# Kernel optimization log

Measured on AMD Instinct MI355X. Metric: run time of the kernel, lower is better.

## Reference

```python
import jax, jax.numpy as jnp
import numpy as np
import math

B, S, DIM = 2, 2048, 1024
H, KVH = 16, 4
HD = DIM // H          # 64, head dim
WINDOW = 256           # sliding-window size (0 = global)
ROPE_BASE = 10000.0
EPS = 1e-6


def setup_inputs() -> dict:
    key = jax.random.key(0)
    ks = jax.random.split(key, 6)
    s = 0.02
    return {
        "x": jax.random.normal(ks[0], (B, S, DIM), jnp.float32),
        "Wq": jax.random.normal(ks[1], (DIM, DIM), jnp.float32) * s,
        "Wk": jax.random.normal(ks[2], (KVH * HD, DIM), jnp.float32) * s,
        "Wv": jax.random.normal(ks[3], (KVH * HD, DIM), jnp.float32) * s,
        "Wo": jax.random.normal(ks[4], (DIM, DIM), jnp.float32) * s,
        "q_gain": jnp.ones((H,), jnp.float32),
        "pair_mix": jnp.tile(jnp.eye(2, dtype=jnp.float32), (H // 2, 1, 1))
                    + 0.01 * jax.random.normal(ks[5], (H // 2, 2, 2), jnp.float32),
    }


def _rms_norm(v):
    # F.rms_norm over last dim, no learned weight
    return v * jax.lax.rsqrt(jnp.mean(v * v, axis=-1, keepdims=True) + EPS)


def _rope_tables(seqlen, dtype):
    inv_freq = 1.0 / (ROPE_BASE ** (jnp.arange(0, HD, 2, dtype=jnp.float32) / HD))  # [HD/2]
    t = jnp.arange(seqlen, dtype=jnp.float32)
    freqs = jnp.outer(t, inv_freq)                        # [S, HD/2]
    return jnp.cos(freqs).astype(dtype)[None, None], jnp.sin(freqs).astype(dtype)[None, None]


def _apply_rotary(v, cos, sin):
    half = v.shape[-1] // 2
    v1, v2 = v[..., :half], v[..., half:]
    return jnp.concatenate((v1 * cos + v2 * sin, -v1 * sin + v2 * cos), axis=-1)


def reference(x, Wq, Wk, Wv, Wo, q_gain, pair_mix):
    bsz, seqlen, dim = x.shape
    q = (x @ Wq.T).reshape(bsz, seqlen, H, HD).transpose(0, 2, 1, 3)    # [B,H,S,D]
    k = (x @ Wk.T).reshape(bsz, seqlen, KVH, HD).transpose(0, 2, 1, 3)  # [B,KV,S,D]
    v = (x @ Wv.T).reshape(bsz, seqlen, KVH, HD).transpose(0, 2, 1, 3)

    q = _rms_norm(q)
    k = _rms_norm(k)
    cos, sin = _rope_tables(seqlen, q.dtype)
    q = _apply_rotary(q, cos, sin)
    k = _apply_rotary(k, cos, sin)
    q = q * q_gain.astype(q.dtype)[None, :, None, None]

    # GQA expansion (repeat_interleave over head axis)
    rep = H // KVH
    k_full = jnp.repeat(k, rep, axis=1)  # [B,H,S,D]
    v_full = jnp.repeat(v, rep, axis=1)

    # sliding-window causal mask: attend iff 0 <= i-j < WINDOW
    pos = jnp.arange(seqlen)
    mask = (pos[:, None] >= pos[None, :]) & (pos[:, None] - pos[None, :] < WINDOW)

    scale = 1.0 / math.sqrt(HD)
    scores = jnp.einsum('bhqd,bhkd->bhqk', q, k_full) * scale
    scores = jnp.where(mask[None, None], scores, jnp.finfo(scores.dtype).min)
    att = jax.nn.softmax(scores, axis=-1)
    y = jnp.einsum('bhqk,bhkd->bhqd', att, v_full)  # [B,H,S,D]

    # paired-head mixing: mix each consecutive head pair with a 2x2 matrix
    yp = y.reshape(bsz, H // 2, 2, seqlen, HD)
    y = jnp.einsum('bpitd,poi->bpotd', yp, pair_mix.astype(y.dtype)).reshape(bsz, H, seqlen, HD)

    out = y.transpose(0, 2, 1, 3).reshape(bsz, seqlen, dim) @ Wo.T
    return out
```

## Files before the change

kernel.cpp:

```cpp
#include <hip/hip_runtime.h>
#include <hip/hip_bf16.h>
#include <cstdint>

#define S_LEN 2048
#define QKV_COLS 1536

typedef __bf16 bf16_t;
typedef bf16_t bf16x8 __attribute__((ext_vector_type(8)));
typedef bf16_t bf16x4 __attribute__((ext_vector_type(4)));
typedef float f32x4 __attribute__((ext_vector_type(4)));

typedef __attribute__((address_space(1))) void as1_void;
typedef __attribute__((address_space(3))) void as3_void;

__device__ __forceinline__ void async_load16(const void* g, void* lds) {
  __builtin_amdgcn_global_load_lds(
      (as1_void*)(uintptr_t)g,
      (as3_void*)(uint32_t)(uintptr_t)lds,
      16, 0, 0);
}

__device__ __forceinline__ uint32_t pkbf(float a, float b) {
  union { bf16_t h[2]; uint32_t u; } c;
  c.h[0] = (bf16_t)a; c.h[1] = (bf16_t)b;
  return c.u;
}

__global__ __launch_bounds__(256) void convert_all(
    const float4* __restrict__ x, const float4* __restrict__ wq,
    const float4* __restrict__ wk, const float4* __restrict__ wv,
    const float4* __restrict__ wo, const float* __restrict__ pm,
    bf16x4* __restrict__ xb, bf16x4* __restrict__ wqkvb, bf16x4* __restrict__ wob) {
  int u = blockIdx.x * 256 + threadIdx.x;
  if (u >= 1441792) {
    int off = u - 1441792;
    int flat = off * 4;
    int row = flat >> 10, colf = flat & 1023;
    int col2p = colf & ~64;
    int p = colf >> 7, ii = (colf >> 6) & 1;
    float4 a = wo[(row * 1024 + col2p) >> 2];
    float4 bq = wo[(row * 1024 + (col2p | 64)) >> 2];
    float m0v = pm[p * 4 + ii], m1v = pm[p * 4 + 2 + ii];
    bf16x4 o4;
    o4[0] = (bf16_t)(m0v * a.x + m1v * bq.x);
    o4[1] = (bf16_t)(m0v * a.y + m1v * bq.y);
    o4[2] = (bf16_t)(m0v * a.z + m1v * bq.z);
    o4[3] = (bf16_t)(m0v * a.w + m1v * bq.w);
    wob[off] = o4;
    return;
  }
  const float4* src; bf16x4* dst; int off;
  if (u < 1048576)      { src = x;  dst = xb;             off = u; }
  else if (u < 1310720) { src = wq; dst = wqkvb;          off = u - 1048576; }
  else if (u < 1376256) { src = wk; dst = wqkvb + 262144; off = u - 1310720; }
  else                  { src = wv; dst = wqkvb + 327680; off = u - 1376256; }
  float4 f = src[off];
  bf16x4 o;
  o[0] = (bf16_t)f.x; o[1] = (bf16_t)f.y; o[2] = (bf16_t)f.z; o[3] = (bf16_t)f.w;
  dst[off] = o;
}

__global__ __launch_bounds__(256) void gemm_qkv(
    const bf16_t* __restrict__ A, const bf16_t* __restrict__ B,
    bf16_t* __restrict__ C, bf16_t* __restrict__ vt,
    const float* __restrict__ q_gain, int N, int K) {
  __shared__ bf16_t As[2][64 * 64];
  __shared__ bf16_t Bs[2][128 * 64];
  const int tid = threadIdx.x;
  const int lane = tid & 63;
  const int w = tid >> 6;
  const int wm = (w & 1) << 5, wn = (w >> 1) << 6;
  const int orig = blockIdx.y * gridDim.x + blockIdx.x;
  const int id = (orig & 7) * 96 + (orig >> 3);
  const int m0 = (id / 12) << 6, n0 = (id % 12) << 7;
  const int fidx = lane & 15, quad = lane >> 4;
  f32x4 acc[2][4] = {};
  int ra0 = (tid + 0) >> 3,   sa0 = ((tid + 0) & 7) ^ (ra0 & 7);
  int ra1 = (tid + 256) >> 3, sa1 = ((tid + 256) & 7) ^ (ra1 & 7);
  const bf16_t* Ag0 = A + (size_t)(m0 + ra0) * K + sa0 * 8;
  const bf16_t* Ag1 = A + (size_t)(m0 + ra1) * K + sa1 * 8;
  const bf16_t* Bg[4];
#pragma unroll
  for (int j = 0; j < 4; j++) {
    int c = tid + j * 256, r = c >> 3, s = (c & 7) ^ (r & 7);
    Bg[j] = B + (size_t)(n0 + r) * K + s * 8;
  }
  int aoff[2][2], boff[4][2];
#pragma unroll
  for (int mi = 0; mi < 2; mi++) {
    int row = wm + mi * 16 + fidx;
#pragma unroll
    for (int half = 0; half < 2; half++)
      aoff[mi][half] = row * 64 + (((half * 4 + quad) ^ (row & 7)) * 8);
  }
#pragma unroll
  for (int ni = 0; ni < 4; ni++) {
    int row = wn + ni * 16 + fidx;
#pragma unroll
    for (int half = 0; half < 2; half++)
      boff[ni][half] = row * 64 + (((half * 4 + quad) ^ (row & 7)) * 8);
  }
  async_load16(Ag0, &As[0][tid * 8]);
  async_load16(Ag1, &As[0][(tid + 256) * 8]);
#pragma unroll
  for (int j = 0; j < 4; j++)
    async_load16(Bg[j], &Bs[0][(tid + j * 256) * 8]);
  int cur = 0;
  for (int kt = 0; kt < K; kt += 64) {
    const int nk = kt + 64;
    if (nk < K) {
      async_load16(Ag0 + nk, &As[cur ^ 1][tid * 8]);
      async_load16(Ag1 + nk, &As[cur ^ 1][(tid + 256) * 8]);
#pragma unroll
      for (int j = 0; j < 4; j++)
        async_load16(Bg[j] + nk, &Bs[cur ^ 1][(tid + j * 256) * 8]);
      asm volatile("s_waitcnt vmcnt(6)" ::: "memory");
    } else {
      asm volatile("s_waitcnt vmcnt(0)" ::: "memory");
    }
    __builtin_amdgcn_s_barrier();
    __builtin_amdgcn_sched_barrier(0);
    bf16x8 af[2][2], bfr[4][2];
#pragma unroll
    for (int mi = 0; mi < 2; mi++)
#pragma unroll
      for (int half = 0; half < 2; half++)
        af[mi][half] = *(const bf16x8*)(&As[cur][aoff[mi][half]]);
#pragma unroll
    for (int ni = 0; ni < 4; ni++)
#pragma unroll
      for (int half = 0; half < 2; half++)
        bfr[ni][half] = *(const bf16x8*)(&Bs[cur][boff[ni][half]]);
#pragma unroll
    for (int half = 0; half < 2; half++)
#pragma unroll
      for (int mi = 0; mi < 2; mi++)
#pragma unroll
        for (int ni = 0; ni < 4; ni++)
          acc[mi][ni] = __builtin_amdgcn_mfma_f32_16x16x32_bf16(
              af[mi][half], bfr[ni][half], acc[mi][ni], 0, 0, 0);
    asm volatile("s_waitcnt lgkmcnt(0)" ::: "memory");
    __builtin_amdgcn_s_barrier();
    cur ^= 1;
  }
  const int hc0 = n0 + wn;
  if (hc0 >= 1280) {
#pragma unroll
    for (int mi = 0; mi < 2; mi++)
#pragma unroll
      for (int ni = 0; ni < 4; ni++) {
        int cg = (hc0 - 1280) + ni * 16 + fidx;
        int g = cg >> 6, dh = cg & 63;
        int srow = m0 + wm + mi * 16 + quad * 4;
        int bb = srow >> 11, si = srow & (S_LEN - 1);
        bf16x4 pack;
#pragma unroll
        for (int r = 0; r < 4; r++) pack[r] = (bf16_t)acc[mi][ni][r];
        *(bf16x4*)(vt + ((size_t)((bb * 4 + g) * 64 + dh)) * S_LEN + si) = pack;
      }
    return;
  }
  float gain = 1.f;
  if (hc0 < 1024) gain = q_gain[hc0 >> 6] * 0.125f;
#pragma unroll
  for (int mi = 0; mi < 2; mi++)
#pragma unroll
    for (int r = 0; r < 4; r++) {
      float ss = 0.f;
#pragma unroll
      for (int ni = 0; ni < 4; ni++) { float t = acc[mi][ni][r]; ss += t * t; }
#pragma unroll
      for (int off = 8; off >= 1; off >>= 1) ss += __shfl_xor(ss, off);
      float scl = rsqrtf(ss * (1.f / 64.f) + 1e-6f);
      int s = (m0 + wm + mi * 16 + quad * 4 + r) & (S_LEN - 1);
#pragma unroll
      for (int ni = 0; ni < 2; ni++) {
        float v1 = acc[mi][ni][r] * scl;
        float v2 = acc[mi][ni + 2][r] * scl;
        float fr = (float)(ni * 16 + fidx);
        float ang = (float)s * __expf(fr * -0.28782313662425575f);
        float sn, cs;
        __sincosf(ang, &sn, &cs);
        acc[mi][ni][r]     = (v1 * cs + v2 * sn) * gain;
        acc[mi][ni + 2][r] = (-v1 * sn + v2 * cs) * gain;
      }
    }
#pragma unroll
  for (int mi = 0; mi < 2; mi++)
#pragma unroll
    for (int ni = 0; ni < 4; ni++)
#pragma unroll
      for (int r = 0; r < 4; r++) {
        int gr = m0 + wm + mi * 16 + quad * 4 + r;
        int gc = n0 + wn + ni * 16 + fidx;
        C[(size_t)gr * N + gc] = (bf16_t)acc[mi][ni][r];
      }
}

__global__ __launch_bounds__(256) void gemm_bt_f32(
    const bf16_t* __restrict__ A, const bf16_t* __restrict__ B,
    float* __restrict__ C, int N, int K) {
  __shared__ bf16_t As[2][64 * 64];
  __shared__ bf16_t Bs[2][128 * 64];
  const int tid = threadIdx.x;
  const int lane = tid & 63;
  const int w = tid >> 6;
  const int wm = (w & 1) << 5, wn = (w >> 1) << 6;
  const int orig = blockIdx.y * gridDim.x + blockIdx.x;
  const int id = (orig & 7) * 64 + (orig >> 3);
  const int m0 = (id >> 3) << 6, n0 = (id & 7) << 7;
  const int fidx = lane & 15, quad = lane >> 4;
  f32x4 acc[2][4] = {};
  int ra0 = (tid + 0) >> 3,   sa0 = ((tid + 0) & 7) ^ (ra0 & 7);
  int ra1 = (tid + 256) >> 3, sa1 = ((tid + 256) & 7) ^ (ra1 & 7);
  const bf16_t* Ag0 = A + (size_t)(m0 + ra0) * K + sa0 * 8;
  const bf16_t* Ag1 = A + (size_t)(m0 + ra1) * K + sa1 * 8;
  const bf16_t* Bg[4];
#pragma unroll
  for (int j = 0; j < 4; j++) {
    int c = tid + j * 256, r = c >> 3, s = (c & 7) ^ (r & 7);
    Bg[j] = B + (size_t)(n0 + r) * K + s * 8;
  }
  int aoff[2][2], boff[4][2];
#pragma unroll
  for (int mi = 0; mi < 2; mi++) {
    int row = wm + mi * 16 + fidx;
#pragma unroll
    for (int half = 0; half < 2; half++)
      aoff[mi][half] = row * 64 + (((half * 4 + quad) ^ (row & 7)) * 8);
  }
#pragma unroll
  for (int ni = 0; ni < 4; ni++) {
    int row = wn + ni * 16 + fidx;
#pragma unroll
    for (int half = 0; half < 2; half++)
      boff[ni][half] = row * 64 + (((half * 4 + quad) ^ (row & 7)) * 8);
  }
  async_load16(Ag0, &As[0][tid * 8]);
  async_load16(Ag1, &As[0][(tid + 256) * 8]);
#pragma unroll
  for (int j = 0; j < 4; j++)
    async_load16(Bg[j], &Bs[0][(tid + j * 256) * 8]);
  int cur = 0;
  for (int kt = 0; kt < K; kt += 64) {
    const int nk = kt + 64;
    if (nk < K) {
      async_load16(Ag0 + nk, &As[cur ^ 1][tid * 8]);
      async_load16(Ag1 + nk, &As[cur ^ 1][(tid + 256) * 8]);
#pragma unroll
      for (int j = 0; j < 4; j++)
        async_load16(Bg[j] + nk, &Bs[cur ^ 1][(tid + j * 256) * 8]);
      asm volatile("s_waitcnt vmcnt(6)" ::: "memory");
    } else {
      asm volatile("s_waitcnt vmcnt(0)" ::: "memory");
    }
    __builtin_amdgcn_s_barrier();
    __builtin_amdgcn_sched_barrier(0);
    bf16x8 af[2][2], bfr[4][2];
#pragma unroll
    for (int mi = 0; mi < 2; mi++)
#pragma unroll
      for (int half = 0; half < 2; half++)
        af[mi][half] = *(const bf16x8*)(&As[cur][aoff[mi][half]]);
#pragma unroll
    for (int ni = 0; ni < 4; ni++)
#pragma unroll
      for (int half = 0; half < 2; half++)
        bfr[ni][half] = *(const bf16x8*)(&Bs[cur][boff[ni][half]]);
#pragma unroll
    for (int half = 0; half < 2; half++)
#pragma unroll
      for (int mi = 0; mi < 2; mi++)
#pragma unroll
        for (int ni = 0; ni < 4; ni++)
          acc[mi][ni] = __builtin_amdgcn_mfma_f32_16x16x32_bf16(
              af[mi][half], bfr[ni][half], acc[mi][ni], 0, 0, 0);
    asm volatile("s_waitcnt lgkmcnt(0)" ::: "memory");
    __builtin_amdgcn_s_barrier();
    cur ^= 1;
  }
#pragma unroll
  for (int mi = 0; mi < 2; mi++)
#pragma unroll
    for (int ni = 0; ni < 4; ni++)
#pragma unroll
      for (int r = 0; r < 4; r++) {
        int gr = m0 + wm + mi * 16 + quad * 4 + r;
        int gc = n0 + wn + ni * 16 + fidx;
        C[(size_t)gr * N + gc] = acc[mi][ni][r];
      }
}

#define FIXMAX 8.0f
#define OST 72
__global__ __launch_bounds__(512) void attn_mfma(
    const bf16_t* __restrict__ qkv, const bf16_t* __restrict__ vt,
    bf16_t* __restrict__ yb) {
  __shared__ f32x4 po[4][2][4][64];
  __shared__ float pps[4][2][64];
  __shared__ bf16_t ob[4][32 * OST];
  const int tid = threadIdx.x, lane = tid & 63, w = tid >> 6;
  const int hw = w & 3, sp = w >> 2;
  const int col = lane & 15, quad = lane >> 4;
  const int orig = blockIdx.z * 256 + blockIdx.y * 64 + blockIdx.x;
  const int id = (orig & 7) * 64 + (orig >> 3);
  const int q0 = (id & 63) * 32, g = (id >> 6) & 3, b = id >> 8;
  const int h = g * 4 + hw;

  bf16x8 qf[2][2];
#pragma unroll
  for (int t = 0; t < 2; t++) {
    const bf16_t* qb =
        qkv + ((size_t)b * S_LEN + q0 + t * 16 + col) * QKV_COLS + h * 64 + quad * 8;
    qf[t][0] = *(const bf16x8*)qb;
    qf[t][1] = *(const bf16x8*)(qb + 32);
  }
  const bf16_t* kbase = qkv + (size_t)b * S_LEN * QKV_COLS + 1024 + g * 64 + quad * 8;
  const bf16_t* vbase = vt + ((size_t)((b * 4 + g) * 64) + col) * S_LEN + quad * 8;

  f32x4 o[2][4] = {};
  float ps[2] = {};

  const int c_lo = max(0, (q0 - 255) >> 5);
  const int c_hi = (q0 + 31) >> 5;
  const int nc = c_hi - c_lo + 1;
  const int c_mid = c_lo + ((nc + 1) >> 1);
  const int my_lo = sp ? c_mid : c_lo;
  const int my_hi = sp ? c_hi : (c_mid - 1);

  for (int c = my_lo; c <= my_hi; c++) {
    const int k0 = c * 32;
    bf16x8 kf[2][2];
#pragma unroll
    for (int nt = 0; nt < 2; nt++) {
      const bf16_t* kp = kbase + (size_t)(k0 + nt * 16 + col) * QKV_COLS;
      kf[nt][0] = *(const bf16x8*)kp;
      kf[nt][1] = *(const bf16x8*)(kp + 32);
    }
    bf16x8 vf[4];
#pragma unroll
    for (int nt2 = 0; nt2 < 4; nt2++)
      vf[nt2] = *(const bf16x8*)(vbase + (size_t)(nt2 * 16) * S_LEN + k0);

#pragma unroll
    for (int t = 0; t < 2; t++) {
      const int qt0 = q0 + t * 16;
      if (k0 > qt0 + 15) continue;
      f32x4 st[2];
#pragma unroll
      for (int nt = 0; nt < 2; nt++) {
        f32x4 a = {};
        a = __builtin_amdgcn_mfma_f32_16x16x32_bf16(kf[nt][0], qf[t][0], a, 0, 0, 0);
        a = __builtin_amdgcn_mfma_f32_16x16x32_bf16(kf[nt][1], qf[t][1], a, 0, 0, 0);
        st[nt] = a;
      }
      const bool needmask = (k0 + 31 > qt0) || (k0 < qt0 - 224);
      float p2[2][4];
      if (needmask) {
        int q = qt0 + col;
#pragma unroll
        for (int nt = 0; nt < 2; nt++)
#pragma unroll
          for (int r = 0; r < 4; r++) {
            int k = k0 + nt * 16 + quad * 4 + r;
            bool valid = (k <= q) && (q - k < 256);
            p2[nt][r] = valid ? __expf(st[nt][r] - FIXMAX) : 0.f;
          }
      } else {
#pragma unroll
        for (int nt = 0; nt < 2; nt++)
#pragma unroll
          for (int r = 0; r < 4; r++)
            p2[nt][r] = __expf(st[nt][r] - FIXMAX);
      }
#pragma unroll
      for (int nt = 0; nt < 2; nt++)
#pragma unroll
        for (int r = 0; r < 4; r++) ps[t] += p2[nt][r];
      uint32_t pk0[2], pk1[2];
      pk0[0] = pkbf(p2[0][0], p2[0][1]); pk0[1] = pkbf(p2[0][2], p2[0][3]);
      pk1[0] = pkbf(p2[1][0], p2[1][1]); pk1[1] = pkbf(p2[1][2], p2[1][3]);
      uint32_t w32[4];
#pragma unroll
      for (int m = 0; m < 4; m++) {
        int srclane = col + 16 * ((2 * quad + (m >> 1)) & 3);
        uint32_t a0 = (uint32_t)__shfl((int)pk0[m & 1], srclane);
        uint32_t a1 = (uint32_t)__shfl((int)pk1[m & 1], srclane);
        w32[m] = (quad < 2) ? a0 : a1;
      }
      union { uint32_t u[4]; bf16x8 v; } pu;
      pu.u[0] = w32[0]; pu.u[1] = w32[1]; pu.u[2] = w32[2]; pu.u[3] = w32[3];
      bf16x8 pf = pu.v;
#pragma unroll
      for (int nt2 = 0; nt2 < 4; nt2++)
        o[t][nt2] = __builtin_amdgcn_mfma_f32_16x16x32_bf16(pf, vf[nt2], o[t][nt2], 0, 0, 0);
    }
  }
  if (sp) {
#pragma unroll
    for (int t = 0; t < 2; t++) {
#pragma unroll
      for (int nt2 = 0; nt2 < 4; nt2++) po[hw][t][nt2][lane] = o[t][nt2];
      pps[hw][t][lane] = ps[t];
    }
  }
  __syncthreads();
  if (sp == 0) {
#pragma unroll
    for (int t = 0; t < 2; t++) {
#pragma unroll
      for (int nt2 = 0; nt2 < 4; nt2++) o[t][nt2] += po[hw][t][nt2][lane];
      ps[t] += pps[hw][t][lane];
    }
#pragma unroll
    for (int t = 0; t < 2; t++) {
      float v = ps[t];
      v += __shfl_xor(v, 16);
      v += __shfl_xor(v, 32);
      float il = 1.f / v;
      float il4[4];
#pragma unroll
      for (int r = 0; r < 4; r++) il4[r] = __shfl(il, quad * 4 + r);
      int row0 = t * 16 + quad * 4;
#pragma unroll
      for (int nt2 = 0; nt2 < 4; nt2++)
#pragma unroll
        for (int r = 0; r < 4; r++)
          ob[hw][(row0 + r) * OST + nt2 * 16 + col] = (bf16_t)(o[t][nt2][r] * il4[r]);
    }
    asm volatile("s_waitcnt lgkmcnt(0)" ::: "memory");
#pragma unroll
    for (int it = 0; it < 4; it++) {
      int row = it * 8 + (lane >> 3);
      int d0 = (lane & 7) * 8;
      bf16x8 v8 = *(const bf16x8*)(ob[hw] + row * OST + d0);
      *(bf16x8*)(yb + ((size_t)b * S_LEN + q0 + row) * 1024 + h * 64 + d0) = v8;
    }
  }
}

extern "C" void kernel_launch(void* const* d_in, const int* in_sizes, int n_in,
                              void* d_out, int out_size, void* d_ws, size_t ws_size,
                              hipStream_t stream) {
  const float* x        = (const float*)d_in[0];
  const float* Wq       = (const float*)d_in[1];
  const float* Wk       = (const float*)d_in[2];
  const float* Wv       = (const float*)d_in[3];
  const float* Wo       = (const float*)d_in[4];
  const float* q_gain   = (const float*)d_in[5];
  const float* pair_mix = (const float*)d_in[6];
  float* out = (float*)d_out;

  bf16_t* ws    = (bf16_t*)d_ws;
  bf16_t* xb    = ws;
  bf16_t* wqkvb = xb + 4096 * 1024;
  bf16_t* wob   = wqkvb + 1536 * 1024;
  bf16_t* qkvb  = wob + 1024 * 1024;
  bf16_t* yb    = qkvb + 4096 * 1536;
  bf16_t* vt    = yb + 4096 * 1024;

  convert_all<<<6656, 256, 0, stream>>>(
      (const float4*)x, (const float4*)Wq, (const float4*)Wk, (const float4*)Wv,
      (const float4*)Wo, pair_mix, (bf16x4*)xb, (bf16x4*)wqkvb, (bf16x4*)wob);
  gemm_qkv<<<dim3(12, 64), 256, 0, stream>>>(xb, wqkvb, qkvb, vt, q_gain, 1536, 1024);
  attn_mfma<<<dim3(64, 4, 2), 512, 0, stream>>>(qkvb, vt, yb);
  gemm_bt_f32<<<dim3(8, 64), 256, 0, stream>>>(yb, wob, out, 1024, 1024);
}
```

Measured before the change: 138.0 us.

## Fuse x fp32-to-bf16 conversion into QKV GEMM A-tile loads

The separate conversion of x to bf16 is removed. The QKV GEMM now reads fp32 x directly into registers, converts it, and writes bf16 into the swizzled LDS tile after the MFMA block, so the next tile's loads overlap compute. This drops a full write and re-read of the bf16 copy of x and shrinks the convert kernel to weights only. In exchange the A tile goes through registers instead of the async direct-to-LDS path, and each GEMM block rereads fp32 x (twice the bytes) once per column tile, which adds register pressure and VMEM traffic.

```diff
diff --git a/kernel.cpp b/kernel.cpp
--- a/kernel.cpp
+++ b/kernel.cpp
@@ -26,14 +26,21 @@
   return c.u;
 }
 
-__global__ __launch_bounds__(256) void convert_all(
-    const float4* __restrict__ x, const float4* __restrict__ wq,
-    const float4* __restrict__ wk, const float4* __restrict__ wv,
-    const float4* __restrict__ wo, const float* __restrict__ pm,
-    bf16x4* __restrict__ xb, bf16x4* __restrict__ wqkvb, bf16x4* __restrict__ wob) {
+__device__ __forceinline__ void cvt_write8(bf16_t* dst, float4 a, float4 b) {
+  bf16x8 v;
+  v[0] = (bf16_t)a.x; v[1] = (bf16_t)a.y; v[2] = (bf16_t)a.z; v[3] = (bf16_t)a.w;
+  v[4] = (bf16_t)b.x; v[5] = (bf16_t)b.y; v[6] = (bf16_t)b.z; v[7] = (bf16_t)b.w;
+  *(bf16x8*)dst = v;
+}
+
+__global__ __launch_bounds__(256) void convert_w(
+    const float4* __restrict__ wq, const float4* __restrict__ wk,
+    const float4* __restrict__ wv, const float4* __restrict__ wo,
+    const float* __restrict__ pm,
+    bf16x4* __restrict__ wqkvb, bf16x4* __restrict__ wob) {
   int u = blockIdx.x * 256 + threadIdx.x;
-  if (u >= 1441792) {
-    int off = u - 1441792;
+  if (u >= 393216) {
+    int off = u - 393216;
     int flat = off * 4;
     int row = flat >> 10, colf = flat & 1023;
     int col2p = colf & ~64;
@@ -50,10 +57,9 @@
     return;
   }
   const float4* src; bf16x4* dst; int off;
-  if (u < 1048576)      { src = x;  dst = xb;             off = u; }
-  else if (u < 1310720) { src = wq; dst = wqkvb;          off = u - 1048576; }
-  else if (u < 1376256) { src = wk; dst = wqkvb + 262144; off = u - 1310720; }
-  else                  { src = wv; dst = wqkvb + 327680; off = u - 1376256; }
+  if (u < 262144)      { src = wq; dst = wqkvb;          off = u; }
+  else if (u < 327680) { src = wk; dst = wqkvb + 262144; off = u - 262144; }
+  else                 { src = wv; dst = wqkvb + 327680; off = u - 327680; }
   float4 f = src[off];
   bf16x4 o;
   o[0] = (bf16_t)f.x; o[1] = (bf16_t)f.y; o[2] = (bf16_t)f.z; o[3] = (bf16_t)f.w;
@@ -61,7 +67,7 @@
 }
 
 __global__ __launch_bounds__(256) void gemm_qkv(
-    const bf16_t* __restrict__ A, const bf16_t* __restrict__ B,
+    const float* __restrict__ Af, const bf16_t* __restrict__ B,
     bf16_t* __restrict__ C, bf16_t* __restrict__ vt,
     const float* __restrict__ q_gain, int N, int K) {
   __shared__ bf16_t As[2][64 * 64];
@@ -77,8 +83,8 @@
   f32x4 acc[2][4] = {};
   int ra0 = (tid + 0) >> 3,   sa0 = ((tid + 0) & 7) ^ (ra0 & 7);
   int ra1 = (tid + 256) >> 3, sa1 = ((tid + 256) & 7) ^ (ra1 & 7);
-  const bf16_t* Ag0 = A + (size_t)(m0 + ra0) * K + sa0 * 8;
-  const bf16_t* Ag1 = A + (size_t)(m0 + ra1) * K + sa1 * 8;
+  const float* Ag0 = Af + (size_t)(m0 + ra0) * K + sa0 * 8;
+  const float* Ag1 = Af + (size_t)(m0 + ra1) * K + sa1 * 8;
   const bf16_t* Bg[4];
 #pragma unroll
   for (int j = 0; j < 4; j++) {
@@ -100,21 +106,31 @@
     for (int half = 0; half < 2; half++)
       boff[ni][half] = row * 64 + (((half * 4 + quad) ^ (row & 7)) * 8);
   }
-  async_load16(Ag0, &As[0][tid * 8]);
-  async_load16(Ag1, &As[0][(tid + 256) * 8]);
-#pragma unroll
-  for (int j = 0; j < 4; j++)
-    async_load16(Bg[j], &Bs[0][(tid + j * 256) * 8]);
+  {
+    float4 a0a = *(const float4*)(Ag0);
+    float4 a0b = *(const float4*)(Ag0 + 4);
+    float4 a1a = *(const float4*)(Ag1);
+    float4 a1b = *(const float4*)(Ag1 + 4);
+#pragma unroll
+    for (int j = 0; j < 4; j++)
+      async_load16(Bg[j], &Bs[0][(tid + j * 256) * 8]);
+    cvt_write8(&As[0][tid * 8], a0a, a0b);
+    cvt_write8(&As[0][(tid + 256) * 8], a1a, a1b);
+    asm volatile("s_waitcnt lgkmcnt(0)" ::: "memory");
+  }
   int cur = 0;
   for (int kt = 0; kt < K; kt += 64) {
     const int nk = kt + 64;
+    float4 a0a, a0b, a1a, a1b;
     if (nk < K) {
-      async_load16(Ag0 + nk, &As[cur ^ 1][tid * 8]);
-      async_load16(Ag1 + nk, &As[cur ^ 1][(tid + 256) * 8]);
+      a0a = *(const float4*)(Ag0 + nk);
+      a0b = *(const float4*)(Ag0 + nk + 4);
+      a1a = *(const float4*)(Ag1 + nk);
+      a1b = *(const float4*)(Ag1 + nk + 4);
 #pragma unroll
       for (int j = 0; j < 4; j++)
         async_load16(Bg[j] + nk, &Bs[cur ^ 1][(tid + j * 256) * 8]);
-      asm volatile("s_waitcnt vmcnt(6)" ::: "memory");
+      asm volatile("s_waitcnt vmcnt(8)" ::: "memory");
     } else {
       asm volatile("s_waitcnt vmcnt(0)" ::: "memory");
     }
@@ -139,6 +155,10 @@
         for (int ni = 0; ni < 4; ni++)
           acc[mi][ni] = __builtin_amdgcn_mfma_f32_16x16x32_bf16(
               af[mi][half], bfr[ni][half], acc[mi][ni], 0, 0, 0);
+    if (nk < K) {
+      cvt_write8(&As[cur ^ 1][tid * 8], a0a, a0b);
+      cvt_write8(&As[cur ^ 1][(tid + 256) * 8], a1a, a1b);
+    }
     asm volatile("s_waitcnt lgkmcnt(0)" ::: "memory");
     __builtin_amdgcn_s_barrier();
     cur ^= 1;
@@ -459,10 +479,10 @@
   bf16_t* yb    = qkvb + 4096 * 1536;
   bf16_t* vt    = yb + 4096 * 1024;
 
-  convert_all<<<6656, 256, 0, stream>>>(
-      (const float4*)x, (const float4*)Wq, (const float4*)Wk, (const float4*)Wv,
-      (const float4*)Wo, pair_mix, (bf16x4*)xb, (bf16x4*)wqkvb, (bf16x4*)wob);
-  gemm_qkv<<<dim3(12, 64), 256, 0, stream>>>(xb, wqkvb, qkvb, vt, q_gain, 1536, 1024);
+  convert_w<<<2560, 256, 0, stream>>>(
+      (const float4*)Wq, (const float4*)Wk, (const float4*)Wv,
+      (const float4*)Wo, pair_mix, (bf16x4*)wqkvb, (bf16x4*)wob);
+  gemm_qkv<<<dim3(12, 64), 256, 0, stream>>>(x, wqkvb, qkvb, vt, q_gain, 1536, 1024);
   attn_mfma<<<dim3(64, 4, 2), 512, 0, stream>>>(qkvb, vt, yb);
   gemm_bt_f32<<<dim3(8, 64), 256, 0, stream>>>(yb, wob, out, 1024, 1024);
 }
```

New measurement: 138.7 us. About the same (+0.5%).
